# Kernel optimization log

Hardware: AMD Instinct MI355X
Metric: run time of the kernel (lower is better)

Reference implementation:

```python
import jax, jax.numpy as jnp
import numpy as np

N = 32768       # total nodes = NUM_GRAPHS * T
F_IN = 32       # num_features
HC = 64         # hidden_channels
HEADS = 4
E = 524288      # edges before self-loops
NUM_GRAPHS = 64 # == batch.max()+1 by construction
T = 512         # time steps per graph (N // NUM_GRAPHS)
OUT = 24        # output_size
NEG_SLOPE = 0.2 # PyG GATConv default


def gat_layer(x, src, dst, W, a_src, a_dst, b, n_nodes):
    """PyG GATConv (concat=True) with edge softmax over incoming edges."""
    H, C = a_src.shape
    h = (x @ W).reshape(n_nodes, H, C)                    # [N,H,C]
    alpha_src = jnp.sum(h * a_src, axis=-1)               # [N,H]
    alpha_dst = jnp.sum(h * a_dst, axis=-1)               # [N,H]
    e = jax.nn.leaky_relu(alpha_src[src] + alpha_dst[dst], NEG_SLOPE)  # [E,H]
    m = jax.ops.segment_max(e, dst, num_segments=n_nodes)
    e = jnp.exp(e - m[dst])
    s = jax.ops.segment_sum(e, dst, num_segments=n_nodes)
    alpha = e / (s[dst] + 1e-16)                          # [E,H]
    msg = h[src] * alpha[..., None]                       # [E,H,C]
    out = jax.ops.segment_sum(msg, dst, num_segments=n_nodes)  # [N,H,C]
    return out.reshape(n_nodes, H * C) + b


def gru_layer(x, Wih, Whh, bih, bhh):
    """torch nn.GRU single layer, batch_first input x: [B,T,Hin] -> ([B,T,H], h_T)."""
    Bsz = x.shape[0]
    H = Whh.shape[1]

    def step(h, xt):
        gi = xt @ Wih.T + bih
        gh = h @ Whh.T + bhh
        ir, iz, inn = jnp.split(gi, 3, axis=-1)
        hr, hz, hn = jnp.split(gh, 3, axis=-1)
        r = jax.nn.sigmoid(ir + hr)
        z = jax.nn.sigmoid(iz + hz)
        n = jnp.tanh(inn + r * hn)
        h_new = (1.0 - z) * n + z * h
        return h_new, h_new

    h0 = jnp.zeros((Bsz, H), x.dtype)
    hT, ys = jax.lax.scan(step, h0, jnp.swapaxes(x, 0, 1))
    return jnp.swapaxes(ys, 0, 1), hT


def setup_inputs() -> dict:
    key = jax.random.key(0)
    ks = jax.random.split(key, 24)
    sc = 0.1
    inp = {
        "x": jax.random.normal(ks[0], (N, F_IN), dtype=jnp.float32),
        "edge_index": jax.random.randint(ks[1], (2, E), 0, N, dtype=jnp.int32),
        "batch": jnp.repeat(jnp.arange(NUM_GRAPHS, dtype=jnp.int32), T),
        # GAT layer 1: F_IN -> HC x HEADS (concat)
        "W1": sc * jax.random.normal(ks[2], (F_IN, HEADS * HC), dtype=jnp.float32),
        "a_src1": sc * jax.random.normal(ks[3], (HEADS, HC), dtype=jnp.float32),
        "a_dst1": sc * jax.random.normal(ks[4], (HEADS, HC), dtype=jnp.float32),
        "b1": jnp.zeros((HEADS * HC,), dtype=jnp.float32),
        # GAT layer 2: HEADS*HC -> HC, 1 head
        "W2": sc * jax.random.normal(ks[5], (HEADS * HC, HC), dtype=jnp.float32),
        "a_src2": sc * jax.random.normal(ks[6], (1, HC), dtype=jnp.float32),
        "a_dst2": sc * jax.random.normal(ks[7], (1, HC), dtype=jnp.float32),
        "b2": jnp.zeros((HC,), dtype=jnp.float32),
        # GRU (2 layers, input_size == hidden_size == HC)
        "gru_Wih0": sc * jax.random.normal(ks[8], (3 * HC, HC), dtype=jnp.float32),
        "gru_Whh0": sc * jax.random.normal(ks[9], (3 * HC, HC), dtype=jnp.float32),
        "gru_bih0": jnp.zeros((3 * HC,), dtype=jnp.float32),
        "gru_bhh0": jnp.zeros((3 * HC,), dtype=jnp.float32),
        "gru_Wih1": sc * jax.random.normal(ks[10], (3 * HC, HC), dtype=jnp.float32),
        "gru_Whh1": sc * jax.random.normal(ks[11], (3 * HC, HC), dtype=jnp.float32),
        "gru_bih1": jnp.zeros((3 * HC,), dtype=jnp.float32),
        "gru_bhh1": jnp.zeros((3 * HC,), dtype=jnp.float32),
        # Linear head
        "Wl": sc * jax.random.normal(ks[12], (OUT, HC), dtype=jnp.float32),
        "bl": jnp.zeros((OUT,), dtype=jnp.float32),
    }
    return inp


def reference(x, edge_index, batch, W1, a_src1, a_dst1, b1, W2, a_src2, a_dst2, b2,
              gru_Wih0, gru_Whh0, gru_bih0, gru_bhh0,
              gru_Wih1, gru_Whh1, gru_bih1, gru_bhh1, Wl, bl):
    # PyG GATConv default add_self_loops=True
    loops = jnp.arange(N, dtype=edge_index.dtype)
    src = jnp.concatenate([edge_index[0], loops])
    dst = jnp.concatenate([edge_index[1], loops])

    h = jax.nn.elu(gat_layer(x, src, dst, W1, a_src1, a_dst1, b1, N))   # [N, HEADS*HC]
    h = jax.nn.elu(gat_layer(h, src, dst, W2, a_src2, a_dst2, b2, N))   # [N, HC]

    # batch is repeat(arange(NUM_GRAPHS), T) so batch.max()+1 == NUM_GRAPHS (static)
    seq = h.reshape(NUM_GRAPHS, T, HC)
    seq, _ = gru_layer(seq, gru_Wih0, gru_Whh0, gru_bih0, gru_bhh0)
    _, hT = gru_layer(seq, gru_Wih1, gru_Whh1, gru_bih1, gru_bhh1)      # [B, HC]
    return hT @ Wl.T + bl                                               # [B, OUT]
```

## Files before the change

### kernel.cpp

```cpp
#include <hip/hip_runtime.h>
#include <hip/hip_bf16.h>

#define N_NODES 32768
#define F_IN    32
#define HC      64
#define HEADS   4
#define NE      524288
#define NET     (NE + N_NODES)
#define NG      64
#define TT      512
#define OUTF    24

__device__ __forceinline__ float lrelu(float x){ return x > 0.f ? x : 0.2f*x; }
__device__ __forceinline__ float eluf (float x){ return x > 0.f ? x : __expf(x)-1.f; }
__device__ __forceinline__ float sigmf(float x){ return 1.f/(1.f+__expf(-x)); }
__device__ __forceinline__ float tanhfast(float x){ return 1.f - 2.f/(__expf(2.f*x)+1.f); }
__device__ __forceinline__ float bcast(float v, int k){
  return __int_as_float(__builtin_amdgcn_readlane(__float_as_int(v), k));
}

__global__ __launch_bounds__(256) void k_deg(const int* __restrict__ ei,
                                             int* __restrict__ deg){
  int e = blockIdx.x*256 + threadIdx.x;
  int d = (e < NE) ? ei[NE+e] : (e - NE);
  atomicAdd(deg + d, 1);
}

__global__ __launch_bounds__(1024) void k_scan(const int* __restrict__ deg,
                                               int* __restrict__ rowptr){
  __shared__ int ps[1024];
  const int t = threadIdx.x;
  const int base = t*32;
  int local[32]; int s = 0;
  #pragma unroll
  for(int i=0;i<32;i++){ local[i]=deg[base+i]; s+=local[i]; }
  ps[t]=s; __syncthreads();
  for(int off=1; off<1024; off<<=1){
    int v = (t>=off) ? ps[t-off] : 0;
    __syncthreads();
    ps[t]+=v;
    __syncthreads();
  }
  int run = (t==0) ? 0 : ps[t-1];
  #pragma unroll
  for(int i=0;i<32;i++){ rowptr[base+i]=run; run+=local[i]; }
  if(t==1023) rowptr[N_NODES]=run;
}

__global__ __launch_bounds__(256) void k_fill(const int* __restrict__ ei,
                                              const int* __restrict__ rowptr,
                                              int* __restrict__ cur,
                                              int* __restrict__ col){
  int e = blockIdx.x*256 + threadIdx.x;
  int s, d;
  if(e < NE){ s = ei[e]; d = ei[NE+e]; } else { s = e-NE; d = s; }
  int pos = atomicAdd(cur + d, 1);
  col[rowptr[d] + pos] = s;
}

__global__ __launch_bounds__(256) void k_alpha1x(const float* __restrict__ x,
                                                 const float* __restrict__ W1,
                                                 const float* __restrict__ a_src,
                                                 const float* __restrict__ a_dst,
                                                 float* __restrict__ as1,
                                                 float* __restrict__ ad1){
  __shared__ float ps[256];
  const int tid = threadIdx.x;
  {
    const int k = tid>>3, q = tid&7;
    const int h = q>>1, isd = q&1;
    const float* av = (isd ? a_dst : a_src) + h*64;
    const float* wr = W1 + k*256 + h*64;
    float acc = 0.f;
    #pragma unroll
    for(int c=0;c<64;c++) acc += wr[c]*av[c];
    ps[(isd?128:0) + k*4 + h] = acc;
  }
  __syncthreads();
  const int n = blockIdx.x*256 + tid;
  const float4* xr = (const float4*)(x + n*32);
  float sa0=0.f,sa1=0.f,sa2=0.f,sa3=0.f, sd0=0.f,sd1=0.f,sd2=0.f,sd3=0.f;
  #pragma unroll
  for(int k4=0;k4<8;k4++){
    float4 v = xr[k4];
    const float* pa = ps + (4*k4)*4;
    const float* pd = ps + 128 + (4*k4)*4;
    sa0 += v.x*pa[0] + v.y*pa[4] + v.z*pa[8]  + v.w*pa[12];
    sa1 += v.x*pa[1] + v.y*pa[5] + v.z*pa[9]  + v.w*pa[13];
    sa2 += v.x*pa[2] + v.y*pa[6] + v.z*pa[10] + v.w*pa[14];
    sa3 += v.x*pa[3] + v.y*pa[7] + v.z*pa[11] + v.w*pa[15];
    sd0 += v.x*pd[0] + v.y*pd[4] + v.z*pd[8]  + v.w*pd[12];
    sd1 += v.x*pd[1] + v.y*pd[5] + v.z*pd[9]  + v.w*pd[13];
    sd2 += v.x*pd[2] + v.y*pd[6] + v.z*pd[10] + v.w*pd[14];
    sd3 += v.x*pd[3] + v.y*pd[7] + v.z*pd[11] + v.w*pd[15];
  }
  *(float4*)(as1+n*4) = make_float4(sa0,sa1,sa2,sa3);
  *(float4*)(ad1+n*4) = make_float4(sd0,sd1,sd2,sd3);
}

__global__ __launch_bounds__(256) void k_gatx(const int* __restrict__ rowptr,
                                              const int* __restrict__ col,
                                              const float* __restrict__ as1,
                                              const float* __restrict__ ad1,
                                              const float* __restrict__ x,
                                              float* __restrict__ agg,
                                              float* __restrict__ s14){
  const int node = blockIdx.x*4 + (threadIdx.x>>6);
  const int lane = threadIdx.x & 63;
  const int h0   = lane>>5;
  const int c    = lane & 31;
  const int beg = rowptr[node], end = rowptr[node+1];
  const float adA = ad1[node*4 + h0];
  const float adB = ad1[node*4 + h0 + 2];
  float accA=0.f, accB=0.f, wsA=0.f, wsB=0.f;
  int j = beg;
  for(; j+3 < end; j += 4){
    int s0 = col[j], s1 = col[j+1], s2 = col[j+2], s3 = col[j+3];
    float4 q0 = *(const float4*)(as1 + s0*4);
    float4 q1 = *(const float4*)(as1 + s1*4);
    float4 q2 = *(const float4*)(as1 + s2*4);
    float4 q3 = *(const float4*)(as1 + s3*4);
    float x0 = x[s0*32 + c];
    float x1 = x[s1*32 + c];
    float x2 = x[s2*32 + c];
    float x3 = x[s3*32 + c];
    float wA0 = __expf(lrelu((h0?q0.y:q0.x) + adA));
    float wA1 = __expf(lrelu((h0?q1.y:q1.x) + adA));
    float wA2 = __expf(lrelu((h0?q2.y:q2.x) + adA));
    float wA3 = __expf(lrelu((h0?q3.y:q3.x) + adA));
    float wB0 = __expf(lrelu((h0?q0.w:q0.z) + adB));
    float wB1 = __expf(lrelu((h0?q1.w:q1.z) + adB));
    float wB2 = __expf(lrelu((h0?q2.w:q2.z) + adB));
    float wB3 = __expf(lrelu((h0?q3.w:q3.z) + adB));
    accA += wA0*x0 + wA1*x1 + wA2*x2 + wA3*x3;
    accB += wB0*x0 + wB1*x1 + wB2*x2 + wB3*x3;
    wsA  += (wA0+wA1) + (wA2+wA3);
    wsB  += (wB0+wB1) + (wB2+wB3);
  }
  for(; j < end; j++){
    int s0 = col[j];
    float4 q0 = *(const float4*)(as1 + s0*4);
    float wA0 = __expf(lrelu((h0?q0.y:q0.x) + adA));
    float wB0 = __expf(lrelu((h0?q0.w:q0.z) + adB));
    float x0 = x[s0*32 + c];
    accA += wA0*x0; accB += wB0*x0;
    wsA += wA0; wsB += wB0;
  }
  agg[node*128 + h0*32 + c]     = accA;
  agg[node*128 + (h0+2)*32 + c] = accB;
  if(c == 0){
    s14[node*4 + h0]     = wsA;
    s14[node*4 + h0 + 2] = wsB;
  }
}

__global__ __launch_bounds__(256) void k_g12(const float* __restrict__ agg,
                                             const float* __restrict__ W1,
                                             const float* __restrict__ s14,
                                             const float* __restrict__ b1,
                                             const float* __restrict__ W2,
                                             const float* __restrict__ a_src2,
                                             const float* __restrict__ a_dst2,
                                             float* __restrict__ h2,
                                             float* __restrict__ as2,
                                             float* __restrict__ ad2){
  __shared__ __align__(16) float ags[32*128];
  __shared__ __align__(16) float o1s[32*256];
  __shared__ float sv[128];
  const int tid  = threadIdx.x;
  const int row0 = blockIdx.x*32;
  const float4* ag = (const float4*)(agg + (size_t)row0*128);
  float4* a4 = (float4*)ags;
  for(int i=tid;i<1024;i+=256) a4[i]=ag[i];
  if(tid<32) ((float4*)sv)[tid]=((const float4*)(s14+row0*4))[tid];
  float wc[32];
  #pragma unroll
  for(int k=0;k<32;k++) wc[k]=W1[k*256+tid];
  const float bb=b1[tid];
  __syncthreads();
  const int h = tid>>6;
  for(int r=0;r<32;r++){
    const float4* ar=(const float4*)(ags + r*128 + h*32);
    float acc=0.f;
    #pragma unroll
    for(int k4=0;k4<8;k4++){
      float4 v=ar[k4];
      acc += v.x*wc[4*k4]+v.y*wc[4*k4+1]+v.z*wc[4*k4+2]+v.w*wc[4*k4+3];
    }
    float inv = 1.f/(sv[r*4+h] + 1e-16f);
    o1s[r*256+tid] = eluf(acc*inv + bb);
  }
  __syncthreads();
  const int c0=(tid&15)*4;
  const int r0=(tid>>4)*2;
  float acc2[2][4]={};
  for(int k=0;k<256;k+=4){
    float wv[4][4];
    #pragma unroll
    for(int i=0;i<4;i++){
      float4 w=*(const float4*)(W2+(k+i)*64+c0);
      wv[i][0]=w.x; wv[i][1]=w.y; wv[i][2]=w.z; wv[i][3]=w.w;
    }
    #pragma unroll
    for(int i=0;i<2;i++){
      float4 xv=*(const float4*)(o1s+(r0+i)*256+k);
      #pragma unroll
      for(int j=0;j<4;j++)
        acc2[i][j]+=xv.x*wv[0][j]+xv.y*wv[1][j]+xv.z*wv[2][j]+xv.w*wv[3][j];
    }
  }
  float* h2s = ags;
  #pragma unroll
  for(int i=0;i<2;i++){
    float4 o = make_float4(acc2[i][0],acc2[i][1],acc2[i][2],acc2[i][3]);
    *(float4*)(h2 + (size_t)(row0+r0+i)*64 + c0) = o;
    *(float4*)(h2s + (r0+i)*64 + c0) = o;
  }
  __syncthreads();
  if(tid < 32){
    const float4* hp=(const float4*)(h2s + tid*64);
    float sa=0.f, sd=0.f;
    #pragma unroll
    for(int i=0;i<16;i++){
      float4 v=hp[i];
      float4 a=((const float4*)a_src2)[i];
      float4 d=((const float4*)a_dst2)[i];
      sa+=v.x*a.x+v.y*a.y+v.z*a.z+v.w*a.w;
      sd+=v.x*d.x+v.y*d.y+v.z*d.z+v.w*d.w;
    }
    as2[row0+tid]=sa; ad2[row0+tid]=sd;
  }
}

__global__ __launch_bounds__(256) void k_gat2(const int* __restrict__ rowptr,
                                              const int* __restrict__ col,
                                              const float* __restrict__ as2,
                                              const float* __restrict__ ad2,
                                              const float* __restrict__ h2,
                                              const float* __restrict__ b2,
                                              float* __restrict__ out2){
  const int node = blockIdx.x*4 + (threadIdx.x>>6);
  const int lane = threadIdx.x & 63;
  const int beg = rowptr[node], end = rowptr[node+1];
  const float ad = ad2[node];
  float acc = 0.f, s = 0.f;
  int j = beg;
  for(; j+3 < end; j += 4){
    int s0 = col[j], s1 = col[j+1], s2 = col[j+2], s3 = col[j+3];
    float a0 = as2[s0], a1 = as2[s1], a2 = as2[s2], a3 = as2[s3];
    float v0 = h2[s0*64+lane], v1 = h2[s1*64+lane];
    float v2 = h2[s2*64+lane], v3 = h2[s3*64+lane];
    float w0 = __expf(lrelu(a0 + ad));
    float w1 = __expf(lrelu(a1 + ad));
    float w2 = __expf(lrelu(a2 + ad));
    float w3 = __expf(lrelu(a3 + ad));
    acc += w0*v0 + w1*v1 + w2*v2 + w3*v3;
    s += (w0+w1) + (w2+w3);
  }
  for(; j < end; j++){
    int s0 = col[j];
    float w0 = __expf(lrelu(as2[s0] + ad));
    acc += w0*h2[s0*64+lane];
    s += w0;
  }
  const float inv = 1.f/(s + 1e-16f);
  out2[node*64+lane] = eluf(acc*inv + b2[lane]);
}

__global__ __launch_bounds__(256) void k_gemm_gi(const float* __restrict__ in,
                                                 const float* __restrict__ Wih,
                                                 const float* __restrict__ bih,
                                                 float* __restrict__ gi){
  __shared__ __align__(16) float xs[64*64];
  __shared__ float wT[64*192];
  const int tid=threadIdx.x;
  const int row0=blockIdx.x*64;
  const float4* xg=(const float4*)(in+row0*64);
  float4* xs4=(float4*)xs;
  for(int i=tid;i<1024;i+=256) xs4[i]=xg[i];
  for(int i=tid;i<12288;i+=256){ wT[(i&63)*192+(i>>6)] = Wih[i]; }
  __syncthreads();
  if(tid<192){
    float wr[64];
    #pragma unroll
    for(int k=0;k<64;k++) wr[k]=wT[k*192+tid];
    const float bj=bih[tid];
    for(int r=0;r<64;r++){
      float acc=bj;
      const float4* xr=(const float4*)(xs+r*64);
      #pragma unroll
      for(int k4=0;k4<16;k4++){
        float4 v=xr[k4];
        acc+=v.x*wr[4*k4]+v.y*wr[4*k4+1]+v.z*wr[4*k4+2]+v.w*wr[4*k4+3];
      }
      gi[(row0+r)*192+tid]=acc;
    }
  }
}

__global__ __launch_bounds__(192,1) void k_gru3(const float* __restrict__ gi1,
                                                const float* __restrict__ Whh0,
                                                const float* __restrict__ bhh0,
                                                const float* __restrict__ Wih1,
                                                const float* __restrict__ bih1,
                                                const float* __restrict__ Whh1,
                                                const float* __restrict__ bhh1,
                                                const float* __restrict__ Wl,
                                                const float* __restrict__ bl,
                                                float* __restrict__ fout){
  __shared__ float h1s[64];
  __shared__ float h2s[64];
  __shared__ float gh1s[192];
  __shared__ float gi2s[192];
  __shared__ float gh2s[192];
  __shared__ float g1r[2][192];
  const int tid  = threadIdx.x;
  const int w    = tid >> 6;
  const int lane = tid & 63;
  const int b    = blockIdx.x;
  const float* gib = gi1 + (size_t)b*TT*192;

  const float* W  = (w==0) ? Whh0 : (w==1) ? Wih1 : Whh1;
  const float* bb = (w==0) ? bhh0 : (w==1) ? bih1 : bhh1;
  float* dst      = (w==0) ? gh1s : (w==1) ? gi2s : gh2s;

  const float4* pa = (const float4*)(W + lane*64);
  const float4* pb = (const float4*)(W + (64+lane)*64);
  const float4* pc = (const float4*)(W + (128+lane)*64);
  float4 Av0=pa[0],  Av1=pa[1],  Av2=pa[2],  Av3=pa[3];
  float4 Av4=pa[4],  Av5=pa[5],  Av6=pa[6],  Av7=pa[7];
  float4 Av8=pa[8],  Av9=pa[9],  AvA=pa[10], AvB=pa[11];
  float4 AvC=pa[12], AvD=pa[13], AvE=pa[14], AvF=pa[15];
  float4 Bv0=pb[0],  Bv1=pb[1],  Bv2=pb[2],  Bv3=pb[3];
  float4 Bv4=pb[4],  Bv5=pb[5],  Bv6=pb[6],  Bv7=pb[7];
  float4 Bv8=pb[8],  Bv9=pb[9],  BvA=pb[10], BvB=pb[11];
  float4 BvC=pb[12], BvD=pb[13], BvE=pb[14], BvF=pb[15];
  float4 Cv0=pc[0],  Cv1=pc[1],  Cv2=pc[2],  Cv3=pc[3];
  float4 Cv4=pc[4],  Cv5=pc[5],  Cv6=pc[6],  Cv7=pc[7];
  float4 Cv8=pc[8],  Cv9=pc[9],  CvA=pc[10], CvB=pc[11];
  float4 CvC=pc[12], CvD=pc[13], CvE=pc[14], CvF=pc[15];
  const float biasA = bb[lane];
  const float biasB = bb[64+lane];
  const float biasC = bb[128+lane];

  float giv0 = 0.f, giv1 = 0.f, giv2 = 0.f;
  if(w == 0){
    g1r[0][lane]     = gib[lane];
    g1r[0][64+lane]  = gib[64+lane];
    g1r[0][128+lane] = gib[128+lane];
    giv0 = gib[192 + lane];
    giv1 = gib[192 + 64+lane];
    giv2 = gib[192 + 128+lane];
  }
  if(tid < 64){ h1s[tid]=0.f; h2s[tid]=0.f; }
  __syncthreads();

  for(int i=0;i<=TT;i++){
    float hv = (w==2) ? h2s[lane] : h1s[lane];
    if(w == 0){
      int pst = i+1;
      if(pst < TT){
        g1r[pst&1][lane]     = giv0;
        g1r[pst&1][64+lane]  = giv1;
        g1r[pst&1][128+lane] = giv2;
      }
      int nst = i+2;
      if(nst < TT){
        giv0 = gib[(size_t)nst*192 + lane];
        giv1 = gib[(size_t)nst*192 + 64+lane];
        giv2 = gib[(size_t)nst*192 + 128+lane];
      }
    }
    float a0=biasA, a1=0.f, a2=0.f, a3=0.f;
    float b0=biasB, b1_=0.f, b2_=0.f, b3=0.f;
    float c0=biasC, c1=0.f, c2=0.f, c3=0.f;
#define DOT4(WA, WB, WC, BASE) { \
    float t0=bcast(hv,BASE+0), t1=bcast(hv,BASE+1), t2=bcast(hv,BASE+2), t3=bcast(hv,BASE+3); \
    a0 = fmaf(t0, WA.x, a0);  b0  = fmaf(t0, WB.x, b0);  c0 = fmaf(t0, WC.x, c0); \
    a1 = fmaf(t1, WA.y, a1);  b1_ = fmaf(t1, WB.y, b1_); c1 = fmaf(t1, WC.y, c1); \
    a2 = fmaf(t2, WA.z, a2);  b2_ = fmaf(t2, WB.z, b2_); c2 = fmaf(t2, WC.z, c2); \
    a3 = fmaf(t3, WA.w, a3);  b3  = fmaf(t3, WB.w, b3);  c3 = fmaf(t3, WC.w, c3); }
    DOT4(Av0,Bv0,Cv0, 0)  DOT4(Av1,Bv1,Cv1, 4)  DOT4(Av2,Bv2,Cv2, 8)  DOT4(Av3,Bv3,Cv3, 12)
    DOT4(Av4,Bv4,Cv4, 16) DOT4(Av5,Bv5,Cv5, 20) DOT4(Av6,Bv6,Cv6, 24) DOT4(Av7,Bv7,Cv7, 28)
    DOT4(Av8,Bv8,Cv8, 32) DOT4(Av9,Bv9,Cv9, 36) DOT4(AvA,BvA,CvA, 40) DOT4(AvB,BvB,CvB, 44)
    DOT4(AvC,BvC,CvC, 48) DOT4(AvD,BvD,CvD, 52) DOT4(AvE,BvE,CvE, 56) DOT4(AvF,BvF,CvF, 60)
#undef DOT4
    dst[lane]     = (a0+a1)+(a2+a3);
    dst[64+lane]  = (b0+b1_)+(b2_+b3);
    dst[128+lane] = (c0+c1)+(c2+c3);
    __syncthreads();
    if(w == 0){
      if(i < TT){
        float r = sigmf(g1r[i&1][lane]     + gh1s[lane]);
        float z = sigmf(g1r[i&1][64+lane]  + gh1s[64+lane]);
        float n = tanhfast(g1r[i&1][128+lane] + r*gh1s[128+lane]);
        h1s[lane] = (1.f-z)*n + z*h1s[lane];
      }
    } else if(w == 2){
      if(i >= 1){
        float r = sigmf(gi2s[lane]     + gh2s[lane]);
        float z = sigmf(gi2s[64+lane]  + gh2s[64+lane]);
        float n = tanhfast(gi2s[128+lane] + r*gh2s[128+lane]);
        h2s[lane] = (1.f-z)*n + z*h2s[lane];
      }
    }
    __syncthreads();
  }

  if(tid < 24){
    float acc = bl[tid];
    const float4* wl4 = (const float4*)(Wl + tid*64);
    #pragma unroll
    for(int k4=0;k4<16;k4++){
      float4 h4 = *(const float4*)(h2s + 4*k4);
      float4 w4 = wl4[k4];
      acc += h4.x*w4.x + h4.y*w4.y + h4.z*w4.z + h4.w*w4.w;
    }
    fout[b*24+tid] = acc;
  }
}

extern "C" void kernel_launch(void* const* d_in, const int* in_sizes, int n_in,
                              void* d_out, int out_size, void* d_ws, size_t ws_size,
                              hipStream_t stream){
  const float* x     =(const float*)d_in[0];
  const int*   ei    =(const int*  )d_in[1];
  const float* W1    =(const float*)d_in[3];
  const float* a_src1=(const float*)d_in[4];
  const float* a_dst1=(const float*)d_in[5];
  const float* b1    =(const float*)d_in[6];
  const float* W2    =(const float*)d_in[7];
  const float* a_src2=(const float*)d_in[8];
  const float* a_dst2=(const float*)d_in[9];
  const float* b2    =(const float*)d_in[10];
  const float* Wih0  =(const float*)d_in[11];
  const float* Whh0  =(const float*)d_in[12];
  const float* bih0  =(const float*)d_in[13];
  const float* bhh0  =(const float*)d_in[14];
  const float* Wih1  =(const float*)d_in[15];
  const float* Whh1  =(const float*)d_in[16];
  const float* bih1  =(const float*)d_in[17];
  const float* bhh1  =(const float*)d_in[18];
  const float* Wl    =(const float*)d_in[19];
  const float* bl    =(const float*)d_in[20];

  float* ws   = (float*)d_ws;
  float* agg  = ws;
  float* s14  = ws + 4194304;
  float* gi   = ws;
  float* out2 = ws + 8388608;
  float* h2   = ws + 16777216;
  float* as1  = ws + 18874368;
  float* ad1  = as1 + 131072;
  float* as2  = ad1 + 131072;
  float* ad2  = as2 + 32768;
  int* rowptr = (int*)(ad2 + 32768);
  int* deg    = rowptr + 32800;
  int* cur    = deg + 32768;
  int* col    = cur + 32768;
  float* fo   = (float*)d_out;

  hipMemsetAsync(deg, 0, 2*32768*sizeof(int), stream);

  k_deg   <<<2176,256,0,stream>>>(ei,deg);
  k_scan  <<<1  ,1024,0,stream>>>(deg,rowptr);
  k_fill  <<<2176,256,0,stream>>>(ei,rowptr,cur,col);

  k_alpha1x<<<128 ,256,0,stream>>>(x,W1,a_src1,a_dst1,as1,ad1);
  k_gatx   <<<8192,256,0,stream>>>(rowptr,col,as1,ad1,x,agg,s14);
  k_g12    <<<1024,256,0,stream>>>(agg,W1,s14,b1,W2,a_src2,a_dst2,h2,as2,ad2);
  k_gat2   <<<8192,256,0,stream>>>(rowptr,col,as2,ad2,h2,b2,out2);
  k_gemm_gi<<<512 ,256,0,stream>>>(out2,Wih0,bih0,gi);
  k_gru3   <<<64  ,192,0,stream>>>(gi,Whh0,bhh0,Wih1,bih1,Whh1,bhh1,Wl,bl,fo);
  (void)in_sizes; (void)n_in; (void)out_size; (void)ws_size;
}
```

Measured before the change: 730.1 us.

## Split GRU recurrent matvec across six waves with K-halves and shared-memory reduction

The sequential GRU kernel now runs 384 threads (six wavefronts) per block instead of 192. Each weight matrix's 64-long dot product is split into two 32-element halves handled by different waves, and the partial sums are added in shared memory before the gate math. The input-gate prefetch is spread over the three extra waves. This halves per-wave FMA work and register-held weights on the latency-bound serial chain, at the cost of extra shared-memory traffic and a larger block synchronising every timestep.

```diff
diff --git a/kernel.cpp b/kernel.cpp
--- a/kernel.cpp
+++ b/kernel.cpp
@@ -298,7 +298,7 @@
   }
 }
 
-__global__ __launch_bounds__(192,1) void k_gru3(const float* __restrict__ gi1,
+__global__ __launch_bounds__(384,1) void k_gru6(const float* __restrict__ gi1,
                                                 const float* __restrict__ Whh0,
                                                 const float* __restrict__ bhh0,
                                                 const float* __restrict__ Wih1,
@@ -310,66 +310,56 @@
                                                 float* __restrict__ fout){
   __shared__ float h1s[64];
   __shared__ float h2s[64];
-  __shared__ float gh1s[192];
-  __shared__ float gi2s[192];
-  __shared__ float gh2s[192];
+  __shared__ float gh1p[2][192];
+  __shared__ float gi2p[2][192];
+  __shared__ float gh2p[2][192];
   __shared__ float g1r[2][192];
   const int tid  = threadIdx.x;
   const int w    = tid >> 6;
   const int lane = tid & 63;
+  const int kh   = (w >= 3) ? 1 : 0;
+  const int m    = (w >= 3) ? (w-3) : w;
   const int b    = blockIdx.x;
   const float* gib = gi1 + (size_t)b*TT*192;
 
-  const float* W  = (w==0) ? Whh0 : (w==1) ? Wih1 : Whh1;
-  const float* bb = (w==0) ? bhh0 : (w==1) ? bih1 : bhh1;
-  float* dst      = (w==0) ? gh1s : (w==1) ? gi2s : gh2s;
-
-  const float4* pa = (const float4*)(W + lane*64);
-  const float4* pb = (const float4*)(W + (64+lane)*64);
-  const float4* pc = (const float4*)(W + (128+lane)*64);
-  float4 Av0=pa[0],  Av1=pa[1],  Av2=pa[2],  Av3=pa[3];
-  float4 Av4=pa[4],  Av5=pa[5],  Av6=pa[6],  Av7=pa[7];
-  float4 Av8=pa[8],  Av9=pa[9],  AvA=pa[10], AvB=pa[11];
-  float4 AvC=pa[12], AvD=pa[13], AvE=pa[14], AvF=pa[15];
-  float4 Bv0=pb[0],  Bv1=pb[1],  Bv2=pb[2],  Bv3=pb[3];
-  float4 Bv4=pb[4],  Bv5=pb[5],  Bv6=pb[6],  Bv7=pb[7];
-  float4 Bv8=pb[8],  Bv9=pb[9],  BvA=pb[10], BvB=pb[11];
-  float4 BvC=pb[12], BvD=pb[13], BvE=pb[14], BvF=pb[15];
-  float4 Cv0=pc[0],  Cv1=pc[1],  Cv2=pc[2],  Cv3=pc[3];
-  float4 Cv4=pc[4],  Cv5=pc[5],  Cv6=pc[6],  Cv7=pc[7];
-  float4 Cv8=pc[8],  Cv9=pc[9],  CvA=pc[10], CvB=pc[11];
-  float4 CvC=pc[12], CvD=pc[13], CvE=pc[14], CvF=pc[15];
-  const float biasA = bb[lane];
-  const float biasB = bb[64+lane];
-  const float biasC = bb[128+lane];
-
-  float giv0 = 0.f, giv1 = 0.f, giv2 = 0.f;
-  if(w == 0){
-    g1r[0][lane]     = gib[lane];
-    g1r[0][64+lane]  = gib[64+lane];
-    g1r[0][128+lane] = gib[128+lane];
-    giv0 = gib[192 + lane];
-    giv1 = gib[192 + 64+lane];
-    giv2 = gib[192 + 128+lane];
+  const float* W  = (m==0) ? Whh0 : (m==1) ? Wih1 : Whh1;
+  const float* bb = (m==0) ? bhh0 : (m==1) ? bih1 : bhh1;
+  float* dst      = (m==0) ? gh1p[kh] : (m==1) ? gi2p[kh] : gh2p[kh];
+
+  const int kof = kh*32;
+  const float4* pa = (const float4*)(W + lane*64       + kof);
+  const float4* pb = (const float4*)(W + (64+lane)*64  + kof);
+  const float4* pc = (const float4*)(W + (128+lane)*64 + kof);
+  float4 Av0=pa[0], Av1=pa[1], Av2=pa[2], Av3=pa[3];
+  float4 Av4=pa[4], Av5=pa[5], Av6=pa[6], Av7=pa[7];
+  float4 Bv0=pb[0], Bv1=pb[1], Bv2=pb[2], Bv3=pb[3];
+  float4 Bv4=pb[4], Bv5=pb[5], Bv6=pb[6], Bv7=pb[7];
+  float4 Cv0=pc[0], Cv1=pc[1], Cv2=pc[2], Cv3=pc[3];
+  float4 Cv4=pc[4], Cv5=pc[5], Cv6=pc[6], Cv7=pc[7];
+  const float biasA = kh ? 0.f : bb[lane];
+  const float biasB = kh ? 0.f : bb[64+lane];
+  const float biasC = kh ? 0.f : bb[128+lane];
+
+  float giv = 0.f;
+  if(w >= 3){
+    const int c = (w-3)*64 + lane;
+    g1r[0][c] = gib[c];
+    giv = gib[192 + c];
   }
   if(tid < 64){ h1s[tid]=0.f; h2s[tid]=0.f; }
   __syncthreads();
 
+  const float* hs = (m==2) ? h2s : h1s;
+  const int hidx = (lane + kof) & 63;
+
   for(int i=0;i<=TT;i++){
-    float hv = (w==2) ? h2s[lane] : h1s[lane];
-    if(w == 0){
+    float hv = hs[hidx];
+    if(w >= 3){
+      const int c = (w-3)*64 + lane;
       int pst = i+1;
-      if(pst < TT){
-        g1r[pst&1][lane]     = giv0;
-        g1r[pst&1][64+lane]  = giv1;
-        g1r[pst&1][128+lane] = giv2;
-      }
+      if(pst < TT) g1r[pst&1][c] = giv;
       int nst = i+2;
-      if(nst < TT){
-        giv0 = gib[(size_t)nst*192 + lane];
-        giv1 = gib[(size_t)nst*192 + 64+lane];
-        giv2 = gib[(size_t)nst*192 + 128+lane];
-      }
+      if(nst < TT) giv = gib[(size_t)nst*192 + c];
     }
     float a0=biasA, a1=0.f, a2=0.f, a3=0.f;
     float b0=biasB, b1_=0.f, b2_=0.f, b3=0.f;
@@ -382,8 +372,6 @@
     a3 = fmaf(t3, WA.w, a3);  b3  = fmaf(t3, WB.w, b3);  c3 = fmaf(t3, WC.w, c3); }
     DOT4(Av0,Bv0,Cv0, 0)  DOT4(Av1,Bv1,Cv1, 4)  DOT4(Av2,Bv2,Cv2, 8)  DOT4(Av3,Bv3,Cv3, 12)
     DOT4(Av4,Bv4,Cv4, 16) DOT4(Av5,Bv5,Cv5, 20) DOT4(Av6,Bv6,Cv6, 24) DOT4(Av7,Bv7,Cv7, 28)
-    DOT4(Av8,Bv8,Cv8, 32) DOT4(Av9,Bv9,Cv9, 36) DOT4(AvA,BvA,CvA, 40) DOT4(AvB,BvB,CvB, 44)
-    DOT4(AvC,BvC,CvC, 48) DOT4(AvD,BvD,CvD, 52) DOT4(AvE,BvE,CvE, 56) DOT4(AvF,BvF,CvF, 60)
 #undef DOT4
     dst[lane]     = (a0+a1)+(a2+a3);
     dst[64+lane]  = (b0+b1_)+(b2_+b3);
@@ -391,16 +379,25 @@
     __syncthreads();
     if(w == 0){
       if(i < TT){
-        float r = sigmf(g1r[i&1][lane]     + gh1s[lane]);
-        float z = sigmf(g1r[i&1][64+lane]  + gh1s[64+lane]);
-        float n = tanhfast(g1r[i&1][128+lane] + r*gh1s[128+lane]);
+        float G0 = gh1p[0][lane]      + gh1p[1][lane];
+        float G1 = gh1p[0][64+lane]   + gh1p[1][64+lane];
+        float G2 = gh1p[0][128+lane]  + gh1p[1][128+lane];
+        float r = sigmf(g1r[i&1][lane]     + G0);
+        float z = sigmf(g1r[i&1][64+lane]  + G1);
+        float n = tanhfast(g1r[i&1][128+lane] + r*G2);
         h1s[lane] = (1.f-z)*n + z*h1s[lane];
       }
     } else if(w == 2){
       if(i >= 1){
-        float r = sigmf(gi2s[lane]     + gh2s[lane]);
-        float z = sigmf(gi2s[64+lane]  + gh2s[64+lane]);
-        float n = tanhfast(gi2s[128+lane] + r*gh2s[128+lane]);
+        float I0 = gi2p[0][lane]      + gi2p[1][lane];
+        float I1 = gi2p[0][64+lane]   + gi2p[1][64+lane];
+        float I2 = gi2p[0][128+lane]  + gi2p[1][128+lane];
+        float G0 = gh2p[0][lane]      + gh2p[1][lane];
+        float G1 = gh2p[0][64+lane]   + gh2p[1][64+lane];
+        float G2 = gh2p[0][128+lane]  + gh2p[1][128+lane];
+        float r = sigmf(I0 + G0);
+        float z = sigmf(I1 + G1);
+        float n = tanhfast(I2 + r*G2);
         h2s[lane] = (1.f-z)*n + z*h2s[lane];
       }
     }
@@ -471,6 +468,6 @@
   k_g12    <<<1024,256,0,stream>>>(agg,W1,s14,b1,W2,a_src2,a_dst2,h2,as2,ad2);
   k_gat2   <<<8192,256,0,stream>>>(rowptr,col,as2,ad2,h2,b2,out2);
   k_gemm_gi<<<512 ,256,0,stream>>>(out2,Wih0,bih0,gi);
-  k_gru3   <<<64  ,192,0,stream>>>(gi,Whh0,bhh0,Wih1,bih1,Whh1,bhh1,Wl,bl,fo);
+  k_gru6   <<<64  ,384,0,stream>>>(gi,Whh0,bhh0,Wih1,bih1,Whh1,bhh1,Wl,bl,fo);
   (void)in_sizes; (void)n_in; (void)out_size; (void)ws_size;
 }
```

Result: no change. 734.7 us (+0.6%).

## Pipeline fused GRU recurrence as three-stage wavefront with one barrier per step

Applied to the files above, without the earlier changes.

The fused two-layer GRU kernel now runs as a three-stage software pipeline across its three waves. Wave 0 runs the layer-0 recurrence, wave 1 computes the layer-1 input projection one step behind, and wave 2 runs the layer-1 recurrence two steps behind. They hand data through double-buffered shared rings, so each step needs one __syncthreads instead of two. Gate math now happens inside each wave with hidden state kept in registers. This shortens the serial critical path per timestep, at the cost of two extra pipeline-fill iterations and a more intricate ring-indexing scheme.

```diff
diff --git a/kernel.cpp b/kernel.cpp
--- a/kernel.cpp
+++ b/kernel.cpp
@@ -298,22 +298,19 @@
   }
 }
 
-__global__ __launch_bounds__(192,1) void k_gru3(const float* __restrict__ gi1,
-                                                const float* __restrict__ Whh0,
-                                                const float* __restrict__ bhh0,
-                                                const float* __restrict__ Wih1,
-                                                const float* __restrict__ bih1,
-                                                const float* __restrict__ Whh1,
-                                                const float* __restrict__ bhh1,
-                                                const float* __restrict__ Wl,
-                                                const float* __restrict__ bl,
-                                                float* __restrict__ fout){
-  __shared__ float h1s[64];
-  __shared__ float h2s[64];
-  __shared__ float gh1s[192];
-  __shared__ float gi2s[192];
-  __shared__ float gh2s[192];
-  __shared__ float g1r[2][192];
+__global__ __launch_bounds__(192,1) void k_gru3r(const float* __restrict__ gi1,
+                                                 const float* __restrict__ Whh0,
+                                                 const float* __restrict__ bhh0,
+                                                 const float* __restrict__ Wih1,
+                                                 const float* __restrict__ bih1,
+                                                 const float* __restrict__ Whh1,
+                                                 const float* __restrict__ bhh1,
+                                                 const float* __restrict__ Wl,
+                                                 const float* __restrict__ bl,
+                                                 float* __restrict__ fout){
+  __shared__ float h1ring[2][64];
+  __shared__ float gi2ring[2][192];
+  __shared__ float h2fin[64];
   const int tid  = threadIdx.x;
   const int w    = tid >> 6;
   const int lane = tid & 63;
@@ -322,7 +319,6 @@
 
   const float* W  = (w==0) ? Whh0 : (w==1) ? Wih1 : Whh1;
   const float* bb = (w==0) ? bhh0 : (w==1) ? bih1 : bhh1;
-  float* dst      = (w==0) ? gh1s : (w==1) ? gi2s : gh2s;
 
   const float4* pa = (const float4*)(W + lane*64);
   const float4* pb = (const float4*)(W + (64+lane)*64);
@@ -343,76 +339,77 @@
   const float biasB = bb[64+lane];
   const float biasC = bb[128+lane];
 
-  float giv0 = 0.f, giv1 = 0.f, giv2 = 0.f;
+  float gc0=0.f,gc1=0.f,gc2=0.f, gn0=0.f,gn1=0.f,gn2=0.f;
   if(w == 0){
-    g1r[0][lane]     = gib[lane];
-    g1r[0][64+lane]  = gib[64+lane];
-    g1r[0][128+lane] = gib[128+lane];
-    giv0 = gib[192 + lane];
-    giv1 = gib[192 + 64+lane];
-    giv2 = gib[192 + 128+lane];
-  }
-  if(tid < 64){ h1s[tid]=0.f; h2s[tid]=0.f; }
-  __syncthreads();
-
-  for(int i=0;i<=TT;i++){
-    float hv = (w==2) ? h2s[lane] : h1s[lane];
-    if(w == 0){
-      int pst = i+1;
-      if(pst < TT){
-        g1r[pst&1][lane]     = giv0;
-        g1r[pst&1][64+lane]  = giv1;
-        g1r[pst&1][128+lane] = giv2;
+    gc0 = gib[lane];       gc1 = gib[64+lane];       gc2 = gib[128+lane];
+    gn0 = gib[192+lane];   gn1 = gib[192+64+lane];   gn2 = gib[192+128+lane];
+  }
+  float h = 0.f;
+  __syncthreads();
+
+  for(int i=0;i<=TT+1;i++){
+    const bool act = (w==0) ? (i < TT) : (w==1) ? (i >= 1 && i <= TT) : (i >= 2);
+    float hv = h;
+    if(w == 1 && act) hv = h1ring[(i-1)&1][lane];
+    float gv0=0.f, gv1=0.f, gv2=0.f;
+    if(w == 2 && act){
+      gv0 = gi2ring[(i-1)&1][lane];
+      gv1 = gi2ring[(i-1)&1][64+lane];
+      gv2 = gi2ring[(i-1)&1][128+lane];
+    }
+    float f0=0.f, f1=0.f, f2=0.f;
+    if(w == 0 && i+2 < TT){
+      const float* g2 = gib + (size_t)(i+2)*192;
+      f0 = g2[lane]; f1 = g2[64+lane]; f2 = g2[128+lane];
+    }
+    if(act){
+      float a0=biasA, a1=0.f, a2=0.f, a3=0.f;
+      float b0=biasB, b1_=0.f, b2_=0.f, b3=0.f;
+      float c0=biasC, c1=0.f, c2=0.f, c3=0.f;
+#define DOT4(WA, WB, WC, BASE) { \
+      float t0=bcast(hv,BASE+0), t1=bcast(hv,BASE+1), t2=bcast(hv,BASE+2), t3=bcast(hv,BASE+3); \
+      a0 = fmaf(t0, WA.x, a0);  b0  = fmaf(t0, WB.x, b0);  c0 = fmaf(t0, WC.x, c0); \
+      a1 = fmaf(t1, WA.y, a1);  b1_ = fmaf(t1, WB.y, b1_); c1 = fmaf(t1, WC.y, c1); \
+      a2 = fmaf(t2, WA.z, a2);  b2_ = fmaf(t2, WB.z, b2_); c2 = fmaf(t2, WC.z, c2); \
+      a3 = fmaf(t3, WA.w, a3);  b3  = fmaf(t3, WB.w, b3);  c3 = fmaf(t3, WC.w, c3); }
+      DOT4(Av0,Bv0,Cv0, 0)  DOT4(Av1,Bv1,Cv1, 4)  DOT4(Av2,Bv2,Cv2, 8)  DOT4(Av3,Bv3,Cv3, 12)
+      DOT4(Av4,Bv4,Cv4, 16) DOT4(Av5,Bv5,Cv5, 20) DOT4(Av6,Bv6,Cv6, 24) DOT4(Av7,Bv7,Cv7, 28)
+      DOT4(Av8,Bv8,Cv8, 32) DOT4(Av9,Bv9,Cv9, 36) DOT4(AvA,BvA,CvA, 40) DOT4(AvB,BvB,CvB, 44)
+      DOT4(AvC,BvC,CvC, 48) DOT4(AvD,BvD,CvD, 52) DOT4(AvE,BvE,CvE, 56) DOT4(AvF,BvF,CvF, 60)
+#undef DOT4
+      float ghA = (a0+a1)+(a2+a3);
+      float ghB = (b0+b1_)+(b2_+b3);
+      float ghC = (c0+c1)+(c2+c3);
+      if(w == 0){
+        float r = sigmf(gc0 + ghA);
+        float z = sigmf(gc1 + ghB);
+        float n = tanhfast(gc2 + r*ghC);
+        h = (1.f-z)*n + z*h;
+        h1ring[i&1][lane] = h;
+        gc0 = gn0; gc1 = gn1; gc2 = gn2;
+        gn0 = f0;  gn1 = f1;  gn2 = f2;
+      } else if(w == 1){
+        gi2ring[i&1][lane]     = ghA;
+        gi2ring[i&1][64+lane]  = ghB;
+        gi2ring[i&1][128+lane] = ghC;
+      } else {
+        float r = sigmf(gv0 + ghA);
+        float z = sigmf(gv1 + ghB);
+        float n = tanhfast(gv2 + r*ghC);
+        h = (1.f-z)*n + z*h;
       }
-      int nst = i+2;
-      if(nst < TT){
-        giv0 = gib[(size_t)nst*192 + lane];
-        giv1 = gib[(size_t)nst*192 + 64+lane];
-        giv2 = gib[(size_t)nst*192 + 128+lane];
-      }
-    }
-    float a0=biasA, a1=0.f, a2=0.f, a3=0.f;
-    float b0=biasB, b1_=0.f, b2_=0.f, b3=0.f;
-    float c0=biasC, c1=0.f, c2=0.f, c3=0.f;
-#define DOT4(WA, WB, WC, BASE) { \
-    float t0=bcast(hv,BASE+0), t1=bcast(hv,BASE+1), t2=bcast(hv,BASE+2), t3=bcast(hv,BASE+3); \
-    a0 = fmaf(t0, WA.x, a0);  b0  = fmaf(t0, WB.x, b0);  c0 = fmaf(t0, WC.x, c0); \
-    a1 = fmaf(t1, WA.y, a1);  b1_ = fmaf(t1, WB.y, b1_); c1 = fmaf(t1, WC.y, c1); \
-    a2 = fmaf(t2, WA.z, a2);  b2_ = fmaf(t2, WB.z, b2_); c2 = fmaf(t2, WC.z, c2); \
-    a3 = fmaf(t3, WA.w, a3);  b3  = fmaf(t3, WB.w, b3);  c3 = fmaf(t3, WC.w, c3); }
-    DOT4(Av0,Bv0,Cv0, 0)  DOT4(Av1,Bv1,Cv1, 4)  DOT4(Av2,Bv2,Cv2, 8)  DOT4(Av3,Bv3,Cv3, 12)
-    DOT4(Av4,Bv4,Cv4, 16) DOT4(Av5,Bv5,Cv5, 20) DOT4(Av6,Bv6,Cv6, 24) DOT4(Av7,Bv7,Cv7, 28)
-    DOT4(Av8,Bv8,Cv8, 32) DOT4(Av9,Bv9,Cv9, 36) DOT4(AvA,BvA,CvA, 40) DOT4(AvB,BvB,CvB, 44)
-    DOT4(AvC,BvC,CvC, 48) DOT4(AvD,BvD,CvD, 52) DOT4(AvE,BvE,CvE, 56) DOT4(AvF,BvF,CvF, 60)
-#undef DOT4
-    dst[lane]     = (a0+a1)+(a2+a3);
-    dst[64+lane]  = (b0+b1_)+(b2_+b3);
-    dst[128+lane] = (c0+c1)+(c2+c3);
+    }
     __syncthreads();
-    if(w == 0){
-      if(i < TT){
-        float r = sigmf(g1r[i&1][lane]     + gh1s[lane]);
-        float z = sigmf(g1r[i&1][64+lane]  + gh1s[64+lane]);
-        float n = tanhfast(g1r[i&1][128+lane] + r*gh1s[128+lane]);
-        h1s[lane] = (1.f-z)*n + z*h1s[lane];
-      }
-    } else if(w == 2){
-      if(i >= 1){
-        float r = sigmf(gi2s[lane]     + gh2s[lane]);
-        float z = sigmf(gi2s[64+lane]  + gh2s[64+lane]);
-        float n = tanhfast(gi2s[128+lane] + r*gh2s[128+lane]);
-        h2s[lane] = (1.f-z)*n + z*h2s[lane];
-      }
-    }
-    __syncthreads();
-  }
-
+  }
+
+  if(w == 2) h2fin[lane] = h;
+  __syncthreads();
   if(tid < 24){
     float acc = bl[tid];
     const float4* wl4 = (const float4*)(Wl + tid*64);
     #pragma unroll
     for(int k4=0;k4<16;k4++){
-      float4 h4 = *(const float4*)(h2s + 4*k4);
+      float4 h4 = *(const float4*)(h2fin + 4*k4);
       float4 w4 = wl4[k4];
       acc += h4.x*w4.x + h4.y*w4.y + h4.z*w4.z + h4.w*w4.w;
     }
@@ -471,6 +468,6 @@
   k_g12    <<<1024,256,0,stream>>>(agg,W1,s14,b1,W2,a_src2,a_dst2,h2,as2,ad2);
   k_gat2   <<<8192,256,0,stream>>>(rowptr,col,as2,ad2,h2,b2,out2);
   k_gemm_gi<<<512 ,256,0,stream>>>(out2,Wih0,bih0,gi);
-  k_gru3   <<<64  ,192,0,stream>>>(gi,Whh0,bhh0,Wih1,bih1,Whh1,bhh1,Wl,bl,fo);
+  k_gru3r  <<<64  ,192,0,stream>>>(gi,Whh0,bhh0,Wih1,bih1,Whh1,bhh1,Wl,bl,fo);
   (void)in_sizes; (void)n_in; (void)out_size; (void)ws_size;
 }
```

After: 732.3 us. No clear change (+0.3%).
